# Optimization experiments

Measured on AMD Instinct MI355X. Metric: run time of the kernel, lower is better.

The kernel has to match this reference:

```python
import jax, jax.numpy as jnp
import numpy as np


def setup_inputs() -> dict:
    key = jax.random.key(0)
    ks = jax.random.split(key, 5)
    B, C, D, H, W = 2, 256, 8, 28, 28
    mid = C // 2
    # Kaiming-normal-ish init (std = sqrt(2/fan_in)) for 1x1 conv weights
    def kaiming(k, shape, fan_in):
        return jax.random.normal(k, shape, dtype=jnp.float32) * np.sqrt(2.0 / fan_in)
    x = jax.random.normal(ks[0], (B, C, D, H, W), dtype=jnp.float32)
    w1 = kaiming(ks[1], (mid, C), C)
    w2 = kaiming(ks[2], (mid, C), C)
    w3 = kaiming(ks[3], (mid, C), C)
    w4 = kaiming(ks[4], (C, mid), mid)
    b1 = jnp.zeros((mid,), jnp.float32)
    b2 = jnp.zeros((mid,), jnp.float32)
    b3 = jnp.zeros((mid,), jnp.float32)
    b4 = jnp.zeros((C,), jnp.float32)
    return {"x": x, "w1": w1, "b1": b1, "w2": w2, "b2": b2,
            "w3": w3, "b3": b3, "w4": w4, "b4": b4}


def reference(x, w1, b1, w2, b2, w3, b3, w4, b4):
    # x: [B, C, D, H, W]; 1x1x1 Conv3d == channel matmul over flattened N = D*H*W
    B, C, D, H, W = x.shape
    N = D * H * W
    xf = x.reshape(B, C, N)                                   # [B, C, N]
    # theta: conv1 -> [B, N, mid]
    e1 = jnp.einsum('mc,bcn->bnm', w1, xf) + b1               # [B, N, mid]
    # phi: conv2 -> [B, mid, N]
    e2 = jnp.einsum('mc,bcn->bmn', w2, xf) + b2[:, None]      # [B, mid, N]
    # g: conv3 -> [B, N, mid]
    e3 = jnp.einsum('mc,bcn->bnm', w3, xf) + b3               # [B, N, mid]
    # unscaled attention: softmax over keys (last axis)
    kernel = jnp.einsum('bnm,bmk->bnk', e1, e2)               # [B, N, N]
    kernel = jax.nn.softmax(kernel, axis=2)
    attn = jnp.einsum('bnk,bkm->bnm', kernel, e3)             # [B, N, mid]
    # conv4 (1x1 Conv1d): mid -> C, applied on [B, mid, N]
    y = jnp.einsum('cm,bnm->bcn', w4, attn) + b4[:, None]     # [B, C, N]
    return x + y.reshape(B, C, D, H, W)
```

## Files before the change

### kernel.cpp

```cpp
#include <hip/hip_runtime.h>


#define BB  2
#define CC  256
#define NN  6272
#define MID 128

typedef _Float16 half4_t __attribute__((ext_vector_type(4)));
typedef _Float16 half8_t __attribute__((ext_vector_type(8)));
typedef float    floatx16 __attribute__((ext_vector_type(16)));

__device__ __forceinline__ void fma4(float4& a, const float4 v, const float s) {
    a.x += v.x * s; a.y += v.y * s; a.z += v.z * s; a.w += v.w * s;
}
__device__ __forceinline__ float dot4(const float4 a, const float4 b) {
    return a.x * b.x + a.y * b.y + a.z * b.z + a.w * b.w;
}

__global__ __launch_bounds__(256, 2) void proj_kernel(
    const float* __restrict__ x,
    const float* __restrict__ w1, const float* __restrict__ bi1,
    const float* __restrict__ w2, const float* __restrict__ bi2,
    const float* __restrict__ w3, const float* __restrict__ bi3,
    _Float16* __restrict__ Qg, _Float16* __restrict__ Kg, _Float16* __restrict__ VtG)
{
    const int t  = threadIdx.x;
    const int n0 = blockIdx.x * 64;
    const int pj = blockIdx.y;
    const int b  = blockIdx.z;
    const float* w  = (pj == 0) ? w1 : (pj == 1) ? w2 : w3;
    const float* bi = (pj == 0) ? bi1 : (pj == 1) ? bi2 : bi3;

    __shared__ float xs[CC * 68];
    {
        const float* xb = x + (size_t)b * CC * NN;
        for (int r = t; r < CC * 16; r += 256) {
            int c = r >> 4, j = (r & 15) << 2;
            float4 v = *(const float4*)(xb + (size_t)c * NN + n0 + j);
            *(float4*)&xs[c * 68 + j] = v;
        }
    }
    __syncthreads();

    const int n4 = (t & 15) << 2;
    const int m0 = (t >> 4) << 3;
    float4 acc4[8];
    #pragma unroll
    for (int k = 0; k < 8; ++k) acc4[k] = make_float4(0.f, 0.f, 0.f, 0.f);

    for (int cc = 0; cc < CC; cc += 4) {
        float4 xv[4];
        #pragma unroll
        for (int u = 0; u < 4; ++u)
            xv[u] = *(const float4*)&xs[(cc + u) * 68 + n4];
        #pragma unroll
        for (int k = 0; k < 8; ++k) {
            float4 wq = *(const float4*)(w + (size_t)(m0 + k) * CC + cc);
            fma4(acc4[k], xv[0], wq.x);
            fma4(acc4[k], xv[1], wq.y);
            fma4(acc4[k], xv[2], wq.z);
            fma4(acc4[k], xv[3], wq.w);
        }
    }

    const float* af = (const float*)acc4;
    float bb[8];
    #pragma unroll
    for (int k = 0; k < 8; ++k) bb[k] = bi[m0 + k];

    if (pj < 2) {
        _Float16* eo = ((pj == 0) ? Qg : Kg) + (size_t)b * NN * MID;
        #pragma unroll
        for (int i = 0; i < 4; ++i) {
            half8_t h;
            #pragma unroll
            for (int k = 0; k < 8; ++k) h[k] = (_Float16)(af[k * 4 + i] + bb[k]);
            *(half8_t*)(eo + (size_t)(n0 + n4 + i) * MID + m0) = h;
        }
    } else {
        _Float16* eo = VtG + (size_t)b * MID * NN;
        #pragma unroll
        for (int k = 0; k < 8; ++k) {
            half4_t h;
            #pragma unroll
            for (int i = 0; i < 4; ++i) h[i] = (_Float16)(af[k * 4 + i] + bb[k]);
            *(half4_t*)(eo + (size_t)(m0 + k) * NN + n0 + n4) = h;
        }
    }
}

__global__ __launch_bounds__(128, 2) void attn_kernel(
    const _Float16* __restrict__ Qg, const _Float16* __restrict__ Kg,
    const _Float16* __restrict__ VtG, float* __restrict__ attnW)
{
    const int t    = threadIdx.x;
    const int lane = t & 63;
    const int wave = t >> 6;
    const int l31  = lane & 31;
    const int l5   = lane >> 5;
    const int q0   = blockIdx.x * 32;
    const int b    = blockIdx.y;

    __shared__ __align__(16) char lds[40960];
    _Float16* Ks = (_Float16*)lds;
    _Float16* Vt = (_Float16*)(lds + 17408);
    _Float16* Pt = (_Float16*)(lds + 17408 + 18432);
    float* stats = (float*)(lds + 40448);
    float* Obuf  = (float*)lds;

    const _Float16* Qb = Qg + ((size_t)b * NN + q0) * MID;
    const _Float16* Kb = Kg + (size_t)b * NN * MID;
    const _Float16* Vb = VtG + (size_t)b * MID * NN;

    half8_t qf[8];
    #pragma unroll
    for (int ds = 0; ds < 8; ++ds)
        qf[ds] = *(const half8_t*)(Qb + (size_t)l31 * MID + ds * 16 + l5 * 8);

    floatx16 o[4];
    #pragma unroll
    for (int dt = 0; dt < 4; ++dt)
        #pragma unroll
        for (int j = 0; j < 16; ++j) o[dt][j] = 0.f;
    float m_run = -3.0e38f, l_run = 0.f;

    for (int kt = 0; kt < NN / 64; ++kt) {
        const int nk = kt * 64;
        #pragma unroll
        for (int it = 0; it < 8; ++it) {
            int c = it * 128 + t;
            int r = c >> 4, off = (c & 15) * 8;
            *(half8_t*)(Ks + r * 136 + off) =
                *(const half8_t*)(Kb + (size_t)(nk + r) * MID + off);
        }
        #pragma unroll
        for (int it = 0; it < 8; ++it) {
            int c = it * 128 + t;
            int d = c >> 3, off = (c & 7) * 8;
            *(half8_t*)(Vt + d * 72 + off) =
                *(const half8_t*)(Vb + (size_t)d * NN + nk + off);
        }
        __syncthreads();

        floatx16 s;
        #pragma unroll
        for (int j = 0; j < 16; ++j) s[j] = 0.f;
        const _Float16* krow = Ks + (wave * 32 + l31) * 136 + l5 * 8;
        #pragma unroll
        for (int ds = 0; ds < 8; ++ds)
            s = __builtin_amdgcn_mfma_f32_32x32x16_f16(
                    *(const half8_t*)(krow + ds * 16), qf[ds], s, 0, 0, 0);

        float tmax = s[0];
        #pragma unroll
        for (int j = 1; j < 16; ++j) tmax = fmaxf(tmax, s[j]);
        tmax = fmaxf(tmax, __shfl_xor(tmax, 32));
        const float m_new = fmaxf(m_run, tmax);
        const float alpha = __expf(m_run - m_new);
        m_run = m_new;

        float psum = 0.f;
        _Float16* prow = Pt + l31 * 72 + wave * 32 + 4 * l5;
        #pragma unroll
        for (int g = 0; g < 4; ++g) {
            float p0 = __expf(s[4 * g + 0] - m_new);
            float p1 = __expf(s[4 * g + 1] - m_new);
            float p2 = __expf(s[4 * g + 2] - m_new);
            float p3 = __expf(s[4 * g + 3] - m_new);
            psum += (p0 + p1) + (p2 + p3);
            half4_t h;
            h[0] = (_Float16)p0; h[1] = (_Float16)p1;
            h[2] = (_Float16)p2; h[3] = (_Float16)p3;
            *(half4_t*)(prow + 8 * g) = h;
        }
        psum += __shfl_xor(psum, 32);
        l_run = l_run * alpha + psum;

        #pragma unroll
        for (int dt = 0; dt < 4; ++dt)
            #pragma unroll
            for (int j = 0; j < 16; ++j) o[dt][j] *= alpha;

        __builtin_amdgcn_s_waitcnt(0xC07F);

        #pragma unroll
        for (int ks = 0; ks < 2; ++ks) {
            half8_t pf = *(const half8_t*)(Pt + l31 * 72 + wave * 32 + ks * 16 + l5 * 8);
            const _Float16* vcol = Vt + wave * 32 + ks * 16 + l5 * 8;
            #pragma unroll
            for (int dt = 0; dt < 4; ++dt)
                o[dt] = __builtin_amdgcn_mfma_f32_32x32x16_f16(
                            *(const half8_t*)(vcol + (dt * 32 + l31) * 72), pf,
                            o[dt], 0, 0, 0);
        }
        __syncthreads();
    }

    if (l5 == 0) {
        stats[wave * 64 + l31]      = m_run;
        stats[wave * 64 + 32 + l31] = l_run;
    }
    __syncthreads();
    const float m_o  = stats[(1 ^ wave) * 64 + l31];
    const float l_o  = stats[(1 ^ wave) * 64 + 32 + l31];
    const float m_st = fmaxf(m_run, m_o);
    const float sc   = __expf(m_run - m_st);
    const float l_st = l_run * sc + l_o * __expf(m_o - m_st);
    const float inv  = 1.0f / l_st;

    if (wave == 1) {
        #pragma unroll
        for (int dt = 0; dt < 4; ++dt)
            #pragma unroll
            for (int j = 0; j < 16; ++j) {
                int d = dt * 32 + (j & 3) + 8 * (j >> 2) + 4 * l5;
                Obuf[l31 * 132 + d] = o[dt][j] * sc;
            }
    }
    __syncthreads();
    if (wave == 0) {
        #pragma unroll
        for (int dt = 0; dt < 4; ++dt)
            #pragma unroll
            for (int j = 0; j < 16; ++j) {
                int d = dt * 32 + (j & 3) + 8 * (j >> 2) + 4 * l5;
                Obuf[l31 * 132 + d] = (Obuf[l31 * 132 + d] + o[dt][j] * sc) * inv;
            }
    }
    __syncthreads();
    #pragma unroll
    for (int it = 0; it < 8; ++it) {
        int c = it * 128 + t;
        int q = c >> 5, off = (c & 31) * 4;
        *(float4*)(attnW + ((size_t)b * NN + q0 + q) * MID + off) =
            *(const float4*)(Obuf + q * 132 + off);
    }
}

__global__ __launch_bounds__(256, 2) void epi_kernel(
    const float* __restrict__ attnW, const float* __restrict__ w4,
    const float* __restrict__ b4, const float* __restrict__ x,
    float* __restrict__ out)
{
    const int t  = threadIdx.x;
    const int n0 = blockIdx.x * 64;
    const int b  = blockIdx.y;

    __shared__ float as[64 * 132];
    for (int r = t; r < 64 * 32; r += 256) {
        int q = r >> 5, g = r & 31;
        float4 v = *(const float4*)(attnW + ((size_t)b * NN + (n0 + q)) * MID + (g << 2));
        *(float4*)&as[q * 132 + (g << 2)] = v;
    }
    __syncthreads();

    const int n4 = (t & 15) << 2;
    const int c0 = (t >> 4) << 4;
    float4 accE[16];
    #pragma unroll
    for (int k = 0; k < 16; ++k) accE[k] = make_float4(0.f, 0.f, 0.f, 0.f);

    for (int ms = 0; ms < 32; ++ms) {
        float4 av[4];
        #pragma unroll
        for (int i = 0; i < 4; ++i)
            av[i] = *(const float4*)&as[(n4 + i) * 132 + (ms << 2)];
        #pragma unroll
        for (int k = 0; k < 16; ++k) {
            float4 wq = *(const float4*)(w4 + (size_t)(c0 + k) * MID + (ms << 2));
            accE[k].x += dot4(av[0], wq);
            accE[k].y += dot4(av[1], wq);
            accE[k].z += dot4(av[2], wq);
            accE[k].w += dot4(av[3], wq);
        }
    }

    #pragma unroll
    for (int k = 0; k < 16; ++k) {
        const int c = c0 + k;
        const float bv = b4[c];
        const size_t off = ((size_t)b * CC + c) * NN + n0 + n4;
        float4 xr = *(const float4*)(x + off);
        float4 r;
        r.x = accE[k].x + bv + xr.x;
        r.y = accE[k].y + bv + xr.y;
        r.z = accE[k].z + bv + xr.z;
        r.w = accE[k].w + bv + xr.w;
        *(float4*)(out + off) = r;
    }
}

extern "C" void kernel_launch(void* const* d_in, const int* in_sizes, int n_in,
                              void* d_out, int out_size, void* d_ws, size_t ws_size,
                              hipStream_t stream)
{
    const float* x  = (const float*)d_in[0];
    const float* w1 = (const float*)d_in[1];
    const float* b1 = (const float*)d_in[2];
    const float* w2 = (const float*)d_in[3];
    const float* b2 = (const float*)d_in[4];
    const float* w3 = (const float*)d_in[5];
    const float* b3 = (const float*)d_in[6];
    const float* w4 = (const float*)d_in[7];
    const float* b4 = (const float*)d_in[8];
    float* out = (float*)d_out;

    _Float16* Qg  = (_Float16*)d_ws;
    _Float16* Kg  = Qg + (size_t)BB * NN * MID;
    _Float16* VtG = Kg + (size_t)BB * NN * MID;
    float* attnW  = (float*)(VtG + (size_t)BB * NN * MID);

    proj_kernel<<<dim3(NN / 64, 3, BB), 256, 0, stream>>>(x, w1, b1, w2, b2, w3, b3, Qg, Kg, VtG);
    attn_kernel<<<dim3(NN / 32, BB), 128, 0, stream>>>(Qg, Kg, VtG, attnW);
    epi_kernel<<<dim3(NN / 64, BB), 256, 0, stream>>>(attnW, w4, b4, x, out);
}
```

Measured before the change: 306.5 us.

## Split attention over key ranges and merge partial outputs in epilogue

The attention kernel now processes 64 queries per 256-thread block, with four waves arranged as 2 query halves by 2 key halves, and the key sequence split four ways across grid.y. Each block writes fp16 partial outputs plus per-row max and sum statistics, which the epilogue merges with softmax rescaling before the output projection. The epilogue grid is also refined to 32 queries by 128 channels per block. The aim is more blocks and better K/V tile reuse per load, at the cost of extra global traffic for the partials and some fp16 rounding of intermediate outputs.

```diff
diff --git a/kernel.cpp b/kernel.cpp
--- a/kernel.cpp
+++ b/kernel.cpp
@@ -5,6 +5,7 @@
 #define CC  256
 #define NN  6272
 #define MID 128
+#define KSPLIT 4
 
 typedef _Float16 half4_t __attribute__((ext_vector_type(4)));
 typedef _Float16 half8_t __attribute__((ext_vector_type(8)));
@@ -89,26 +90,34 @@
     }
 }
 
-__global__ __launch_bounds__(128, 2) void attn_kernel(
+__global__ __launch_bounds__(256, 3) void attn_kernel(
     const _Float16* __restrict__ Qg, const _Float16* __restrict__ Kg,
-    const _Float16* __restrict__ VtG, float* __restrict__ attnW)
+    const _Float16* __restrict__ VtG, _Float16* __restrict__ Opart,
+    float* __restrict__ Mst, float* __restrict__ Lst)
 {
     const int t    = threadIdx.x;
     const int lane = t & 63;
     const int wave = t >> 6;
+    const int qh   = wave & 1;
+    const int kh   = wave >> 1;
     const int l31  = lane & 31;
     const int l5   = lane >> 5;
-    const int q0   = blockIdx.x * 32;
-    const int b    = blockIdx.y;
-
-    __shared__ __align__(16) char lds[40960];
+    const int q0   = blockIdx.x * 64;
+    const int split= blockIdx.y;
+    const int b    = blockIdx.z;
+
+    const int t0   = split * 24 + (split < 2 ? split : 2);
+    const int tcnt = (split < 2) ? 25 : 24;
+
+    __shared__ __align__(16) char lds[46208];
     _Float16* Ks = (_Float16*)lds;
     _Float16* Vt = (_Float16*)(lds + 17408);
-    _Float16* Pt = (_Float16*)(lds + 17408 + 18432);
-    float* stats = (float*)(lds + 40448);
+    _Float16* Pt = (_Float16*)(lds + 35840);
+    float* msh   = (float*)(lds + 45056);
+    float* lsh   = msh + 144;
     float* Obuf  = (float*)lds;
 
-    const _Float16* Qb = Qg + ((size_t)b * NN + q0) * MID;
+    const _Float16* Qb = Qg + ((size_t)b * NN + q0 + qh * 32) * MID;
     const _Float16* Kb = Kg + (size_t)b * NN * MID;
     const _Float16* Vb = VtG + (size_t)b * MID * NN;
 
@@ -124,18 +133,18 @@
         for (int j = 0; j < 16; ++j) o[dt][j] = 0.f;
     float m_run = -3.0e38f, l_run = 0.f;
 
-    for (int kt = 0; kt < NN / 64; ++kt) {
+    for (int kt = t0; kt < t0 + tcnt; ++kt) {
         const int nk = kt * 64;
         #pragma unroll
-        for (int it = 0; it < 8; ++it) {
-            int c = it * 128 + t;
+        for (int it = 0; it < 4; ++it) {
+            int c = it * 256 + t;
             int r = c >> 4, off = (c & 15) * 8;
             *(half8_t*)(Ks + r * 136 + off) =
                 *(const half8_t*)(Kb + (size_t)(nk + r) * MID + off);
         }
         #pragma unroll
-        for (int it = 0; it < 8; ++it) {
-            int c = it * 128 + t;
+        for (int it = 0; it < 4; ++it) {
+            int c = it * 256 + t;
             int d = c >> 3, off = (c & 7) * 8;
             *(half8_t*)(Vt + d * 72 + off) =
                 *(const half8_t*)(Vb + (size_t)d * NN + nk + off);
@@ -145,7 +154,7 @@
         floatx16 s;
         #pragma unroll
         for (int j = 0; j < 16; ++j) s[j] = 0.f;
-        const _Float16* krow = Ks + (wave * 32 + l31) * 136 + l5 * 8;
+        const _Float16* krow = Ks + (kh * 32 + l31) * 136 + l5 * 8;
         #pragma unroll
         for (int ds = 0; ds < 8; ++ds)
             s = __builtin_amdgcn_mfma_f32_32x32x16_f16(
@@ -160,7 +169,7 @@
         m_run = m_new;
 
         float psum = 0.f;
-        _Float16* prow = Pt + l31 * 72 + wave * 32 + 4 * l5;
+        _Float16* prow = Pt + (qh * 32 + l31) * 72 + kh * 32 + 4 * l5;
         #pragma unroll
         for (int g = 0; g < 4; ++g) {
             float p0 = __expf(s[4 * g + 0] - m_new);
@@ -185,8 +194,9 @@
 
         #pragma unroll
         for (int ks = 0; ks < 2; ++ks) {
-            half8_t pf = *(const half8_t*)(Pt + l31 * 72 + wave * 32 + ks * 16 + l5 * 8);
-            const _Float16* vcol = Vt + wave * 32 + ks * 16 + l5 * 8;
+            half8_t pf = *(const half8_t*)(Pt + (qh * 32 + l31) * 72 +
+                                           kh * 32 + ks * 16 + l5 * 8);
+            const _Float16* vcol = Vt + kh * 32 + ks * 16 + l5 * 8;
             #pragma unroll
             for (int dt = 0; dt < 4; ++dt)
                 o[dt] = __builtin_amdgcn_mfma_f32_32x32x16_f16(
@@ -196,69 +206,111 @@
         __syncthreads();
     }
 
-    if (l5 == 0) {
-        stats[wave * 64 + l31]      = m_run;
-        stats[wave * 64 + 32 + l31] = l_run;
-    }
-    __syncthreads();
-    const float m_o  = stats[(1 ^ wave) * 64 + l31];
-    const float l_o  = stats[(1 ^ wave) * 64 + 32 + l31];
-    const float m_st = fmaxf(m_run, m_o);
-    const float sc   = __expf(m_run - m_st);
-    const float l_st = l_run * sc + l_o * __expf(m_o - m_st);
-    const float inv  = 1.0f / l_st;
-
-    if (wave == 1) {
+    const int qm = qh * 32 + l31;
+    if (l5 == 0) { msh[kh * 72 + qm] = m_run; lsh[kh * 72 + qm] = l_run; }
+    __syncthreads();
+    const float m0v = msh[qm], m1v = msh[72 + qm];
+    const float M   = fmaxf(m0v, m1v);
+    const float Lt  = lsh[qm] * __expf(m0v - M) + lsh[72 + qm] * __expf(m1v - M);
+    const float sc  = __expf(m_run - M) / Lt;
+
+    if (kh == 0) {
         #pragma unroll
         for (int dt = 0; dt < 4; ++dt)
             #pragma unroll
             for (int j = 0; j < 16; ++j) {
                 int d = dt * 32 + (j & 3) + 8 * (j >> 2) + 4 * l5;
-                Obuf[l31 * 132 + d] = o[dt][j] * sc;
+                Obuf[qm * 132 + d] = o[dt][j] * sc;
             }
     }
     __syncthreads();
-    if (wave == 0) {
+    if (kh == 1) {
         #pragma unroll
         for (int dt = 0; dt < 4; ++dt)
             #pragma unroll
             for (int j = 0; j < 16; ++j) {
                 int d = dt * 32 + (j & 3) + 8 * (j >> 2) + 4 * l5;
-                Obuf[l31 * 132 + d] = (Obuf[l31 * 132 + d] + o[dt][j] * sc) * inv;
+                Obuf[qm * 132 + d] += o[dt][j] * sc;
             }
     }
     __syncthreads();
-    #pragma unroll
-    for (int it = 0; it < 8; ++it) {
-        int c = it * 128 + t;
-        int q = c >> 5, off = (c & 31) * 4;
-        *(float4*)(attnW + ((size_t)b * NN + q0 + q) * MID + off) =
-            *(const float4*)(Obuf + q * 132 + off);
+
+    _Float16* Ob = Opart + ((size_t)(b * KSPLIT + split) * NN + q0) * MID;
+    #pragma unroll
+    for (int it = 0; it < 4; ++it) {
+        int c = it * 256 + t;
+        int q = c >> 4, off = (c & 15) * 8;
+        half8_t h;
+        #pragma unroll
+        for (int j = 0; j < 8; ++j) h[j] = (_Float16)Obuf[q * 132 + off + j];
+        *(half8_t*)(Ob + (size_t)q * MID + off) = h;
+    }
+    if (t < 64) {
+        const float a0 = msh[t], a1 = msh[72 + t];
+        const float MM = fmaxf(a0, a1);
+        const float LL = lsh[t] * __expf(a0 - MM) + lsh[72 + t] * __expf(a1 - MM);
+        const size_t idx = (size_t)(b * KSPLIT + split) * NN + q0 + t;
+        Mst[idx] = MM;
+        Lst[idx] = LL;
     }
 }
 
 __global__ __launch_bounds__(256, 2) void epi_kernel(
-    const float* __restrict__ attnW, const float* __restrict__ w4,
+    const _Float16* __restrict__ Opart, const float* __restrict__ Mst,
+    const float* __restrict__ Lst, const float* __restrict__ w4,
     const float* __restrict__ b4, const float* __restrict__ x,
     float* __restrict__ out)
 {
     const int t  = threadIdx.x;
-    const int n0 = blockIdx.x * 64;
-    const int b  = blockIdx.y;
-
-    __shared__ float as[64 * 132];
-    for (int r = t; r < 64 * 32; r += 256) {
-        int q = r >> 5, g = r & 31;
-        float4 v = *(const float4*)(attnW + ((size_t)b * NN + (n0 + q)) * MID + (g << 2));
-        *(float4*)&as[q * 132 + (g << 2)] = v;
-    }
-    __syncthreads();
-
-    const int n4 = (t & 15) << 2;
-    const int c0 = (t >> 4) << 4;
-    float4 accE[16];
-    #pragma unroll
-    for (int k = 0; k < 16; ++k) accE[k] = make_float4(0.f, 0.f, 0.f, 0.f);
+    const int n0 = blockIdx.x * 32;
+    const int ch = blockIdx.y;
+    const int b  = blockIdx.z;
+
+    __shared__ float as[32 * 132];
+    __shared__ float wts[KSPLIT][36];
+
+    if (t < 32) {
+        float m[KSPLIT], l[KSPLIT];
+        #pragma unroll
+        for (int s = 0; s < KSPLIT; ++s) {
+            const size_t idx = (size_t)(b * KSPLIT + s) * NN + n0 + t;
+            m[s] = Mst[idx]; l[s] = Lst[idx];
+        }
+        float M = m[0];
+        #pragma unroll
+        for (int s = 1; s < KSPLIT; ++s) M = fmaxf(M, m[s]);
+        float L = 0.f, wl[KSPLIT];
+        #pragma unroll
+        for (int s = 0; s < KSPLIT; ++s) { wl[s] = l[s] * __expf(m[s] - M); L += wl[s]; }
+        const float inv = 1.0f / L;
+        #pragma unroll
+        for (int s = 0; s < KSPLIT; ++s) wts[s][t] = wl[s] * inv;
+    }
+    __syncthreads();
+
+    for (int r = t; r < 32 * 16; r += 256) {
+        int q = r >> 4, off = (r & 15) * 8;
+        float acc[8];
+        #pragma unroll
+        for (int j = 0; j < 8; ++j) acc[j] = 0.f;
+        #pragma unroll
+        for (int s = 0; s < KSPLIT; ++s) {
+            const float wv = wts[s][q];
+            half8_t h = *(const half8_t*)(Opart +
+                ((size_t)(b * KSPLIT + s) * NN + n0 + q) * MID + off);
+            #pragma unroll
+            for (int j = 0; j < 8; ++j) acc[j] += wv * (float)h[j];
+        }
+        *(float4*)&as[q * 132 + off]     = make_float4(acc[0], acc[1], acc[2], acc[3]);
+        *(float4*)&as[q * 132 + off + 4] = make_float4(acc[4], acc[5], acc[6], acc[7]);
+    }
+    __syncthreads();
+
+    const int n4 = (t & 7) << 2;
+    const int c0 = ch * 128 + (t >> 3) * 4;
+    float4 accE[4];
+    #pragma unroll
+    for (int k = 0; k < 4; ++k) accE[k] = make_float4(0.f, 0.f, 0.f, 0.f);
 
     for (int ms = 0; ms < 32; ++ms) {
         float4 av[4];
@@ -266,7 +318,7 @@
         for (int i = 0; i < 4; ++i)
             av[i] = *(const float4*)&as[(n4 + i) * 132 + (ms << 2)];
         #pragma unroll
-        for (int k = 0; k < 16; ++k) {
+        for (int k = 0; k < 4; ++k) {
             float4 wq = *(const float4*)(w4 + (size_t)(c0 + k) * MID + (ms << 2));
             accE[k].x += dot4(av[0], wq);
             accE[k].y += dot4(av[1], wq);
@@ -276,7 +328,7 @@
     }
 
     #pragma unroll
-    for (int k = 0; k < 16; ++k) {
+    for (int k = 0; k < 4; ++k) {
         const int c = c0 + k;
         const float bv = b4[c];
         const size_t off = ((size_t)b * CC + c) * NN + n0 + n4;
@@ -305,12 +357,14 @@
     const float* b4 = (const float*)d_in[8];
     float* out = (float*)d_out;
 
-    _Float16* Qg  = (_Float16*)d_ws;
-    _Float16* Kg  = Qg + (size_t)BB * NN * MID;
-    _Float16* VtG = Kg + (size_t)BB * NN * MID;
-    float* attnW  = (float*)(VtG + (size_t)BB * NN * MID);
+    _Float16* Qg    = (_Float16*)d_ws;
+    _Float16* Kg    = Qg + (size_t)BB * NN * MID;
+    _Float16* VtG   = Kg + (size_t)BB * NN * MID;
+    _Float16* Opart = VtG + (size_t)BB * NN * MID;
+    float*    Mst   = (float*)(Opart + (size_t)BB * KSPLIT * NN * MID);
+    float*    Lst   = Mst + (size_t)BB * KSPLIT * NN;
 
     proj_kernel<<<dim3(NN / 64, 3, BB), 256, 0, stream>>>(x, w1, b1, w2, b2, w3, b3, Qg, Kg, VtG);
-    attn_kernel<<<dim3(NN / 32, BB), 128, 0, stream>>>(Qg, Kg, VtG, attnW);
-    epi_kernel<<<dim3(NN / 64, BB), 256, 0, stream>>>(attnW, w4, b4, x, out);
-}
+    attn_kernel<<<dim3(NN / 64, KSPLIT, BB), 256, 0, stream>>>(Qg, Kg, VtG, Opart, Mst, Lst);
+    epi_kernel<<<dim3(NN / 32, 2, BB), 256, 0, stream>>>(Opart, Mst, Lst, w4, b4, x, out);
+}
```

Measured after the change: 311.5 us. Within noise of the previous version (+1.6%).
